# Kernel optimization log

Measured on AMD Instinct MI355X. Metric: run time of the kernel, lower is better.

The kernel has to match this reference:

```python
import jax, jax.numpy as jnp
import numpy as np

BN_EPS = 1e-5


def gcn_conv(x, src, dst, n, W, b):
    # PyG GCNConv: h = x @ W; add self-loops; symmetric deg^{-1/2} norm; scatter-add; + bias
    h = x @ W
    sl = jnp.arange(n, dtype=src.dtype)
    src_f = jnp.concatenate([src, sl])
    dst_f = jnp.concatenate([dst, sl])
    deg = jax.ops.segment_sum(jnp.ones_like(dst_f, dtype=h.dtype), dst_f, num_segments=n)
    dis = jnp.where(deg > 0, jax.lax.rsqrt(jnp.maximum(deg, 1.0)), 0.0)
    norm = dis[src_f] * dis[dst_f]                       # [E+N]
    msg = h[src_f] * norm[:, None]                       # gather + scale
    out = jax.ops.segment_sum(msg, dst_f, num_segments=n)  # scatter-add
    return out + b


def batchnorm(x, g, b):
    # training-mode BatchNorm1d (batch statistics), deterministic
    mu = jnp.mean(x, axis=0)
    var = jnp.mean((x - mu) ** 2, axis=0)
    return g * (x - mu) * jax.lax.rsqrt(var + BN_EPS) + b


def setup_inputs() -> dict:
    key = jax.random.key(0)
    ks = jax.random.split(key, 12)
    N, E, F_IN, D, M, G = 40000, 640000, 128, 128, 256, 2000
    x = jax.random.normal(ks[0], (N, F_IN), dtype=jnp.float32)
    edge_index = jax.random.randint(ks[1], (2, E), 0, N, dtype=jnp.int64)
    batch = jnp.sort(jax.random.randint(ks[2], (N,), 0, G, dtype=jnp.int64))
    s = lambda fi: 1.0 / np.sqrt(fi)
    W1 = jax.random.normal(ks[3], (F_IN, D), dtype=jnp.float32) * s(F_IN)
    b1 = jnp.zeros((D,), jnp.float32)
    W2 = jax.random.normal(ks[4], (D, D), dtype=jnp.float32) * s(D)
    b2 = jnp.zeros((D,), jnp.float32)
    bn1_g = jnp.ones((D,), jnp.float32); bn1_b = jnp.zeros((D,), jnp.float32)
    bn2_g = jnp.ones((D,), jnp.float32); bn2_b = jnp.zeros((D,), jnp.float32)
    fc1_w = jax.random.normal(ks[5], (D, M), dtype=jnp.float32) * s(D)
    fc1_b = jnp.zeros((M,), jnp.float32)
    fc2_w = jax.random.normal(ks[6], (M, M), dtype=jnp.float32) * s(M)
    fc2_b = jnp.zeros((M,), jnp.float32)
    fc3_w = jax.random.normal(ks[7], (M, 1), dtype=jnp.float32) * s(M)
    fc3_b = jnp.zeros((1,), jnp.float32)
    return dict(x=x, edge_index=edge_index, batch=batch, num_graphs=G,
                W1=W1, b1=b1, W2=W2, b2=b2,
                bn1_g=bn1_g, bn1_b=bn1_b, bn2_g=bn2_g, bn2_b=bn2_b,
                fc1_w=fc1_w, fc1_b=fc1_b, fc2_w=fc2_w, fc2_b=fc2_b,
                fc3_w=fc3_w, fc3_b=fc3_b)


def reference(x, edge_index, batch, num_graphs, W1, b1, W2, b2,
              bn1_g, bn1_b, bn2_g, bn2_b,
              fc1_w, fc1_b, fc2_w, fc2_b, fc3_w, fc3_b):
    n = x.shape[0]
    src, dst = edge_index[0], edge_index[1]
    h = gcn_conv(x, src, dst, n, W1, b1)
    h = jax.nn.relu(batchnorm(h, bn1_g, bn1_b))
    h = gcn_conv(h, src, dst, n, W2, b2)
    h = jax.nn.relu(batchnorm(h, bn2_g, bn2_b))
    g = jax.ops.segment_sum(h, batch, num_segments=num_graphs)  # scatter_sum pooling [G, D]
    g = jax.nn.relu(g @ fc1_w + fc1_b)   # dropout is identity in eval
    g = jax.nn.relu(g @ fc2_w + fc2_b)
    return g @ fc3_w + fc3_b             # [G, 1]
```

## Files before the change

kernel.cpp:

```cpp
#include <hip/hip_runtime.h>
#include <hip/hip_fp16.h>

#define NN 40000
#define NE 640000
#define DF 128
#define NG 2000
#define NCH 157
#define FILLB 625
#define G1_BLKS 313
#define NCHUNK 64
#define ECH 10000
#define NOCT 8
#define QN 5120
#define NPAD (NOCT * QN)
#define NWIN 160
#define HISTB (NCHUNK * NOCT)

typedef unsigned int u32;
typedef __attribute__((ext_vector_type(8))) short short8;
typedef __attribute__((ext_vector_type(4))) float floatx4;

__device__ inline float2 bf2_to_f2(u32 u) {
    return make_float2(__uint_as_float(u << 16), __uint_as_float(u & 0xffff0000u));
}
__device__ inline u32 f_to_bf(float f) {
    u32 u = __float_as_uint(f);
    return (u + 0x7fffu + ((u >> 16) & 1u)) >> 16;
}
__device__ inline u32 pack_bf2(float a, float b) {
    return f_to_bf(a) | (f_to_bf(b) << 16);
}
__device__ inline float bf_to_f(short s) {
    return __uint_as_float(((u32)(unsigned short)s) << 16);
}
__device__ inline float colw_to_f(int cw) {
    return __half2float(__ushort_as_half((unsigned short)((u32)cw >> 16)));
}

template<bool BF16IN, bool FUSE_BN, bool WT_F32, bool TILE128>
__device__ __forceinline__ void gemm_core(const void* __restrict__ Xv, const void* __restrict__ wsrc,
                                          u32* __restrict__ outb, const float* __restrict__ slots,
                                          const float* __restrict__ gam, const float* __restrict__ bet,
                                          int bid, char* sbuf, float* sc, float* sh) {
    unsigned short* wlds = (unsigned short*)sbuf;
    unsigned short* clds = (unsigned short*)sbuf;
    int tid = threadIdx.x;
    int row0 = bid * (TILE128 ? 128 : 64);

    if (FUSE_BN) {
        if (tid < 128) {
            float s = 0.f, q = 0.f;
            for (int k = 0; k < 64; k++) {
                s += slots[k * 256 + tid];
                q += slots[k * 256 + 128 + tid];
            }
            const float inv_n = 1.0f / (float)NN;
            float mu = s * inv_n;
            float va = fmaf(-mu, mu, q * inv_n);
            float a = gam[tid] * rsqrtf(va + 1e-5f);
            sc[tid] = a;
            sh[tid] = fmaf(-mu, a, bet[tid]);
        }
    }
    if (WT_F32) {
        const float* W = (const float*)wsrc;
        for (int i = tid; i < 16384; i += 256) {
            int k = i >> 7, c = i & 127;
            wlds[c * 136 + k] = (unsigned short)f_to_bf(W[i]);
        }
    } else {
        const unsigned short* wt = (const unsigned short*)wsrc;
        for (int i = tid; i < 2048; i += 256) {
            int c = i >> 4, s = i & 15;
            *(uint4*)&wlds[c * 136 + s * 8] = ((const uint4*)wt)[i];
        }
    }
    __syncthreads();

    int lane = tid & 63;
    int wave = tid >> 6;
    int qr = lane >> 4;
    int rl = lane & 15;

    if (TILE128) {
        int rA0 = row0 + wave * 32 + rl;
        int rA1 = rA0 + 16;
        int rA0c = rA0 < NN ? rA0 : NN - 1;
        int rA1c = rA1 < NN ? rA1 : NN - 1;
        floatx4 acc[2][8];
#pragma unroll
        for (int a = 0; a < 2; a++)
#pragma unroll
            for (int b = 0; b < 8; b++) acc[a][b] = (floatx4){0.f, 0.f, 0.f, 0.f};
#pragma unroll
        for (int kb = 0; kb < 4; kb++) {
            int k0 = kb * 32 + qr * 8;
            short8 a0, a1;
            if (!BF16IN) {
                const float* p0 = (const float*)Xv + (size_t)rA0c * DF + k0;
                const float* p1 = (const float*)Xv + (size_t)rA1c * DF + k0;
                float4 u0 = *(const float4*)p0, u1 = *(const float4*)(p0 + 4);
                float4 v0 = *(const float4*)p1, v1 = *(const float4*)(p1 + 4);
                float fa[8] = {u0.x, u0.y, u0.z, u0.w, u1.x, u1.y, u1.z, u1.w};
                float fb[8] = {v0.x, v0.y, v0.z, v0.w, v1.x, v1.y, v1.z, v1.w};
#pragma unroll
                for (int j = 0; j < 8; j++) { a0[j] = (short)f_to_bf(fa[j]); a1[j] = (short)f_to_bf(fb[j]); }
            } else {
                a0 = *(const short8*)((const u32*)Xv + (size_t)rA0c * 64 + (k0 >> 1));
                a1 = *(const short8*)((const u32*)Xv + (size_t)rA1c * 64 + (k0 >> 1));
                if (FUSE_BN) {
#pragma unroll
                    for (int j = 0; j < 8; j++) {
                        float f0 = fmaxf(fmaf(bf_to_f(a0[j]), sc[k0 + j], sh[k0 + j]), 0.f);
                        float f1 = fmaxf(fmaf(bf_to_f(a1[j]), sc[k0 + j], sh[k0 + j]), 0.f);
                        a0[j] = (short)f_to_bf(f0);
                        a1[j] = (short)f_to_bf(f1);
                    }
                }
            }
#pragma unroll
            for (int ct = 0; ct < 8; ct++) {
                short8 bfr = *(const short8*)&wlds[(ct * 16 + rl) * 136 + k0];
                acc[0][ct] = __builtin_amdgcn_mfma_f32_16x16x32_bf16(a0, bfr, acc[0][ct], 0, 0, 0);
                acc[1][ct] = __builtin_amdgcn_mfma_f32_16x16x32_bf16(a1, bfr, acc[1][ct], 0, 0, 0);
            }
        }
        __syncthreads();
#pragma unroll
        for (int rt = 0; rt < 2; rt++)
#pragma unroll
            for (int ct = 0; ct < 8; ct++)
#pragma unroll
                for (int r = 0; r < 4; r++) {
                    int lr = wave * 32 + rt * 16 + qr * 4 + r;
                    int c = ct * 16 + rl;
                    clds[lr * 136 + c] = (unsigned short)f_to_bf(acc[rt][ct][r]);
                }
        __syncthreads();
        for (int i = tid; i < 2048; i += 256) {
            int lr = i >> 4, s = i & 15;
            int grow = row0 + lr;
            if (grow < NN) {
                uint4 v = *(const uint4*)&clds[lr * 136 + s * 8];
                ((uint4*)(outb + (size_t)grow * 64))[s] = v;
            }
        }
    } else {
        int rA = row0 + wave * 16 + rl;
        floatx4 acc[8];
#pragma unroll
        for (int b = 0; b < 8; b++) acc[b] = (floatx4){0.f, 0.f, 0.f, 0.f};
#pragma unroll
        for (int kb = 0; kb < 4; kb++) {
            int k0 = kb * 32 + qr * 8;
            short8 a0;
            if (!BF16IN) {
                const float* p0 = (const float*)Xv + (size_t)rA * DF + k0;
                float4 u0 = *(const float4*)p0, u1 = *(const float4*)(p0 + 4);
                float fa[8] = {u0.x, u0.y, u0.z, u0.w, u1.x, u1.y, u1.z, u1.w};
#pragma unroll
                for (int j = 0; j < 8; j++) a0[j] = (short)f_to_bf(fa[j]);
            } else {
                a0 = *(const short8*)((const u32*)Xv + (size_t)rA * 64 + (k0 >> 1));
                if (FUSE_BN) {
#pragma unroll
                    for (int j = 0; j < 8; j++) {
                        float f0 = fmaxf(fmaf(bf_to_f(a0[j]), sc[k0 + j], sh[k0 + j]), 0.f);
                        a0[j] = (short)f_to_bf(f0);
                    }
                }
            }
#pragma unroll
            for (int ct = 0; ct < 8; ct++) {
                short8 bfr = *(const short8*)&wlds[(ct * 16 + rl) * 136 + k0];
                acc[ct] = __builtin_amdgcn_mfma_f32_16x16x32_bf16(a0, bfr, acc[ct], 0, 0, 0);
            }
        }
        __syncthreads();
#pragma unroll
        for (int ct = 0; ct < 8; ct++)
#pragma unroll
            for (int r = 0; r < 4; r++) {
                int lr = wave * 16 + qr * 4 + r;
                int c = ct * 16 + rl;
                clds[lr * 136 + c] = (unsigned short)f_to_bf(acc[ct][r]);
            }
        __syncthreads();
        for (int i = tid; i < 1024; i += 256) {
            int lr = i >> 4, s = i & 15;
            uint4 v = *(const uint4*)&clds[lr * 136 + s * 8];
            ((uint4*)(outb + (size_t)(row0 + lr) * 64))[s] = v;
        }
    }
}

__global__ __launch_bounds__(256, 4) void k_countgemm(const int* __restrict__ dst,
                                                      int* __restrict__ degT, int* __restrict__ rank,
                                                      int* __restrict__ wsum, float* __restrict__ slots0,
                                                      const float* __restrict__ W1, const float* __restrict__ W2,
                                                      unsigned short* __restrict__ wt2,
                                                      const float* __restrict__ X, u32* __restrict__ outb) {
    __shared__ __align__(16) char sbuf[34816];
    __shared__ float sc[128], sh[128];
    int bid = blockIdx.x;
    int tid = threadIdx.x;
    if (bid < HISTB) {
        int c = bid >> 3, oct = bid & 7;
        int nlo = oct * QN;
        int* hist = (int*)sbuf;
        for (int i = tid; i < QN; i += 256) hist[i] = 0;
        __syncthreads();
        int ebase = c * ECH;
        for (int i = tid; i < ECH; i += 256) {
            int d = dst[ebase + i];
            int t = d - nlo;
            if ((u32)t < (u32)QN) rank[ebase + i] = atomicAdd(&hist[t], 1);
        }
        __syncthreads();
        for (int i = tid; i < QN; i += 256) degT[(size_t)c * NPAD + nlo + i] = hist[i];
        int wv = tid >> 6, lane = tid & 63;
        for (int lw = wv; lw < 20; lw += 4) {
            int v = hist[lw * 256 + lane] + hist[lw * 256 + 64 + lane]
                  + hist[lw * 256 + 128 + lane] + hist[lw * 256 + 192 + lane];
            for (int off = 32; off > 0; off >>= 1) v += __shfl_down(v, off);
            if (lane == 0) wsum[c * NWIN + oct * 20 + lw] = v;
        }
        return;
    }
    if (bid < HISTB + 2) {
        float* s = slots0 + (size_t)(bid - HISTB) * 64 * 256;
        for (int i = tid; i < 64 * 256; i += 256) s[i] = 0.f;
        return;
    }
    if (bid == HISTB + 2) {
        for (int i = tid; i < 128 * 128; i += 256) {
            int k = i >> 7, cc = i & 127;
            wt2[cc * 128 + k] = (unsigned short)f_to_bf(W2[i]);
        }
        return;
    }
    gemm_core<false, false, true, true>(X, W1, outb, nullptr, nullptr, nullptr,
                                        bid - HISTB - 3, sbuf, sc, sh);
}

__global__ __launch_bounds__(256) void k_scan(const int* __restrict__ degT, const int* __restrict__ wsum,
                                              int* __restrict__ baseT,
                                              int* __restrict__ row_ptr, float* __restrict__ dis) {
    __shared__ int red[256];
    __shared__ int ls[256];
    int tid = threadIdx.x;
    int wnd = blockIdx.x;
    int part = 0;
    int wp = tid < NWIN ? tid : tid - NWIN;
    for (int idx = tid; idx < NCHUNK * NWIN; idx += 256) {
        if (wp < wnd) part += wsum[idx];
        wp += 96; if (wp >= NWIN) wp -= NWIN;
    }
    red[tid] = part;
    int n = wnd * 256 + tid;
    int run = 0;
#pragma unroll 4
    for (int c = 0; c < NCHUNK; c++) {
        int v = degT[(size_t)c * NPAD + n];
        baseT[(size_t)c * NPAD + n] = run;
        run += v;
    }
    int d = run;
    ls[tid] = d;
    __syncthreads();
#pragma unroll
    for (int off = 128; off > 0; off >>= 1) {
        if (tid < off) red[tid] += red[tid + off];
        __syncthreads();
    }
    int base = red[0];
#pragma unroll
    for (int off = 1; off < 256; off <<= 1) {
        int t = (tid >= off) ? ls[tid - off] : 0;
        __syncthreads();
        ls[tid] += t;
        __syncthreads();
    }
    if (n < NN) {
        int r = base + ls[tid] - d;
        row_ptr[n] = r;
        dis[n] = rsqrtf((float)(d + 1));
    }
    if (wnd == NCH - 1 && tid == 0) row_ptr[NN] = NE;
}

__global__ __launch_bounds__(256) void k_fill(const int* __restrict__ src, const int* __restrict__ dst,
                                              const int* __restrict__ rank, const int* __restrict__ row_ptr,
                                              const int* __restrict__ baseT,
                                              const float* __restrict__ dis, u32* __restrict__ col) {
    int e0 = blockIdx.x * 1024 + threadIdx.x;
#pragma unroll
    for (int q = 0; q < 4; q++) {
        int e = e0 + q * 256;
        int d = dst[e];
        int s = src[e];
        int r = rank[e];
        int c = e / ECH;
        u32 h = (u32)__half_as_ushort(__float2half(dis[s]));
        col[row_ptr[d] + baseT[(size_t)c * NPAD + d] + r] = (u32)s | (h << 16);
    }
}

__global__ __launch_bounds__(256, 4) void k_gemm2(const u32* __restrict__ Hb, const unsigned short* __restrict__ wt2,
                                                  u32* __restrict__ outb, const float* __restrict__ slots,
                                                  const float* __restrict__ gam, const float* __restrict__ bet) {
    __shared__ __align__(16) char sbuf[34816];
    __shared__ float sc[128], sh[128];
    gemm_core<true, true, false, true>(Hb, wt2, outb, slots, gam, bet, blockIdx.x, sbuf, sc, sh);
}

__global__ __launch_bounds__(256, 8) void k_gather(const u32* __restrict__ Hb, const int* __restrict__ row_ptr,
                                                   const u32* __restrict__ col, const float* __restrict__ dis,
                                                   const float* __restrict__ bias, u32* __restrict__ outb,
                                                   float* __restrict__ slots) {
    __shared__ float sred[4][128];
    __shared__ float qred[4][128];
    int t = threadIdx.x & 63;
    int wv = threadIdx.x >> 6;
    int node = blockIdx.x * 4 + wv;
    float di = dis[node];
    int lo = row_ptr[node], hi = row_ptr[node + 1];
    float2 acc;
    {
        float2 a = bf2_to_f2(Hb[(size_t)node * 64 + t]);
        float s = di * di;
        acc = make_float2(a.x * s, a.y * s);
    }
    for (int base = lo; base < hi; base += 64) {
        int m = hi - base; if (m > 64) m = 64;
        int cw = 0;
        if (t < m) cw = (int)col[base + t];
        int ng = (m + 3) >> 2;
        int c[4]; u32 u[4];
#pragma unroll
        for (int q = 0; q < 4; q++) {
            int idx = q < m ? q : 0;
            c[q] = __shfl(cw, idx);
            u[q] = Hb[(size_t)(c[q] & 0xffff) * 64 + t];
        }
        for (int g = 1; g < ng; g++) {
            int c2[4]; u32 u2[4];
#pragma unroll
            for (int q = 0; q < 4; q++) {
                int ii = g * 4 + q;
                int idx = ii < m ? ii : 0;
                c2[q] = __shfl(cw, idx);
                u2[q] = Hb[(size_t)(c2[q] & 0xffff) * 64 + t];
            }
#pragma unroll
            for (int q = 0; q < 4; q++) {
                int ii = (g - 1) * 4 + q;
                float wq = ii < m ? di * colw_to_f(c[q]) : 0.f;
                float2 h = bf2_to_f2(u[q]);
                acc.x = fmaf(h.x, wq, acc.x);
                acc.y = fmaf(h.y, wq, acc.y);
            }
#pragma unroll
            for (int q = 0; q < 4; q++) { c[q] = c2[q]; u[q] = u2[q]; }
        }
#pragma unroll
        for (int q = 0; q < 4; q++) {
            int ii = (ng - 1) * 4 + q;
            float wq = ii < m ? di * colw_to_f(c[q]) : 0.f;
            float2 h = bf2_to_f2(u[q]);
            acc.x = fmaf(h.x, wq, acc.x);
            acc.y = fmaf(h.y, wq, acc.y);
        }
    }
    float2 b = ((const float2*)bias)[t];
    acc.x += b.x; acc.y += b.y;
    outb[(size_t)node * 64 + t] = pack_bf2(acc.x, acc.y);
    sred[wv][2 * t] = acc.x;     sred[wv][2 * t + 1] = acc.y;
    qred[wv][2 * t] = acc.x * acc.x; qred[wv][2 * t + 1] = acc.y * acc.y;
    __syncthreads();
    int tid = threadIdx.x;
    if (tid < 128) {
        float s = sred[0][tid] + sred[1][tid] + sred[2][tid] + sred[3][tid];
        float q = qred[0][tid] + qred[1][tid] + qred[2][tid] + qred[3][tid];
        int slot = blockIdx.x & 63;
        atomicAdd(&slots[slot * 256 + tid], s);
        atomicAdd(&slots[slot * 256 + 128 + tid], q);
    }
}

__global__ __launch_bounds__(256) void k_poolfc(const u32* __restrict__ Hb, const int* __restrict__ batch,
                                                const float* __restrict__ slots,
                                                const float* __restrict__ gam, const float* __restrict__ bet,
                                                const float* __restrict__ fc1w, const float* __restrict__ fc1b,
                                                const float* __restrict__ fc2w, const float* __restrict__ fc2b,
                                                const float* __restrict__ fc3w, const float* __restrict__ fc3b,
                                                float* __restrict__ out) {
    __shared__ float sc[128], sh[128];
    __shared__ float pooled[4][128];
    __shared__ float g1[4][256];
    __shared__ float g2[4][256];
    __shared__ int bnds[5];
    int tid = threadIdx.x;
    int gbase = blockIdx.x * 4;
    if (tid < 128) {
        float s = 0.f, q = 0.f;
        for (int k = 0; k < 64; k++) {
            s += slots[k * 256 + tid];
            q += slots[k * 256 + 128 + tid];
        }
        const float inv_n = 1.0f / (float)NN;
        float mu = s * inv_n;
        float va = fmaf(-mu, mu, q * inv_n);
        float a = gam[tid] * rsqrtf(va + 1e-5f);
        sc[tid] = a;
        sh[tid] = fmaf(-mu, a, bet[tid]);
    } else if (tid < 133) {
        int target = gbase + (tid - 128);
        int a = 0, b = NN;
        while (a < b) { int m = (a + b) >> 1; if (batch[m] < target) a = m + 1; else b = m; }
        bnds[tid - 128] = a;
    }
    __syncthreads();
    {
        int g = tid >> 6, p = tid & 63;
        int lo = bnds[g], hi = bnds[g + 1];
        float a0 = 0.f, a1 = 0.f;
        float sc0 = sc[2 * p], sh0 = sh[2 * p], sc1 = sc[2 * p + 1], sh1 = sh[2 * p + 1];
        for (int i = lo; i < hi; i++) {
            float2 v = bf2_to_f2(Hb[(size_t)i * 64 + p]);
            a0 += fmaxf(fmaf(v.x, sc0, sh0), 0.f);
            a1 += fmaxf(fmaf(v.y, sc1, sh1), 0.f);
        }
        pooled[g][2 * p] = a0;
        pooled[g][2 * p + 1] = a1;
    }
    __syncthreads();
    {
        float x0 = 0.f, x1 = 0.f, x2 = 0.f, x3 = 0.f;
        for (int k = 0; k < 128; k++) {
            float wv = fc1w[k * 256 + tid];
            x0 = fmaf(pooled[0][k], wv, x0);
            x1 = fmaf(pooled[1][k], wv, x1);
            x2 = fmaf(pooled[2][k], wv, x2);
            x3 = fmaf(pooled[3][k], wv, x3);
        }
        float bb = fc1b[tid];
        g1[0][tid] = fmaxf(x0 + bb, 0.f);
        g1[1][tid] = fmaxf(x1 + bb, 0.f);
        g1[2][tid] = fmaxf(x2 + bb, 0.f);
        g1[3][tid] = fmaxf(x3 + bb, 0.f);
    }
    __syncthreads();
    {
        float x0 = 0.f, x1 = 0.f, x2 = 0.f, x3 = 0.f;
        for (int k = 0; k < 256; k++) {
            float wv = fc2w[k * 256 + tid];
            x0 = fmaf(g1[0][k], wv, x0);
            x1 = fmaf(g1[1][k], wv, x1);
            x2 = fmaf(g1[2][k], wv, x2);
            x3 = fmaf(g1[3][k], wv, x3);
        }
        float bb = fc2b[tid];
        g2[0][tid] = fmaxf(x0 + bb, 0.f);
        g2[1][tid] = fmaxf(x1 + bb, 0.f);
        g2[2][tid] = fmaxf(x2 + bb, 0.f);
        g2[3][tid] = fmaxf(x3 + bb, 0.f);
    }
    __syncthreads();
    {
        int lane = tid & 63, wv = tid >> 6;
        float s = fmaf(g2[wv][lane], fc3w[lane],
                  fmaf(g2[wv][64 + lane], fc3w[64 + lane],
                  fmaf(g2[wv][128 + lane], fc3w[128 + lane],
                       g2[wv][192 + lane] * fc3w[192 + lane])));
        for (int off = 32; off > 0; off >>= 1) s += __shfl_down(s, off);
        if (lane == 0) out[gbase + wv] = s + fc3b[0];
    }
}

extern "C" void kernel_launch(void* const* d_in, const int* in_sizes, int n_in,
                              void* d_out, int out_size, void* d_ws, size_t ws_size,
                              hipStream_t stream) {
    const float* x    = (const float*)d_in[0];
    const int*   ei   = (const int*)d_in[1];
    const int*   batch= (const int*)d_in[2];
    const float* W1   = (const float*)d_in[4];
    const float* b1   = (const float*)d_in[5];
    const float* W2   = (const float*)d_in[6];
    const float* b2   = (const float*)d_in[7];
    const float* bn1g = (const float*)d_in[8];
    const float* bn1b = (const float*)d_in[9];
    const float* bn2g = (const float*)d_in[10];
    const float* bn2b = (const float*)d_in[11];
    const float* fc1w = (const float*)d_in[12];
    const float* fc1b = (const float*)d_in[13];
    const float* fc2w = (const float*)d_in[14];
    const float* fc2b = (const float*)d_in[15];
    const float* fc3w = (const float*)d_in[16];
    const float* fc3b = (const float*)d_in[17];
    const int* src = ei;
    const int* dst = ei + NE;
    float* outp = (float*)d_out;

    char* w = (char*)d_ws;
    size_t o = 0;
    auto alloc = [&](size_t bytes) -> char* {
        char* p = w + o;
        o = (o + bytes + 255) & ~(size_t)255;
        return p;
    };
    int*   degT    = (int*)alloc((size_t)NCHUNK * NPAD * 4);
    int*   baseT   = (int*)alloc((size_t)NCHUNK * NPAD * 4);
    int*   wsum    = (int*)alloc((size_t)NCHUNK * NWIN * 4);
    float* slots0  = (float*)alloc((size_t)2 * 64 * 256 * 4);
    int*   row_ptr = (int*)alloc((size_t)(NN + 1) * 4);
    int*   rank    = (int*)alloc((size_t)NE * 4);
    u32*   col     = (u32*)alloc((size_t)NE * 4);
    float* dis     = (float*)alloc((size_t)NN * 4);
    unsigned short* wt2 = (unsigned short*)alloc(128 * 128 * 2);
    u32*   bufA    = (u32*)alloc((size_t)NN * 64 * 4);
    u32*   bufB    = (u32*)alloc((size_t)NN * 64 * 4);
    float* slotsA  = slots0;
    float* slotsB  = slots0 + 64 * 256;

    k_countgemm<<<HISTB + 3 + G1_BLKS, 256, 0, stream>>>(dst, degT, rank, wsum, slots0,
                                                         W1, W2, wt2, x, bufA);
    k_scan<<<NCH, 256, 0, stream>>>(degT, wsum, baseT, row_ptr, dis);
    k_fill<<<FILLB, 256, 0, stream>>>(src, dst, rank, row_ptr, baseT, dis, col);
    k_gather<<<NN / 4, 256, 0, stream>>>(bufA, row_ptr, col, dis, b1, bufB, slotsA);
    k_gemm2<<<G1_BLKS, 256, 0, stream>>>(bufB, wt2, bufA, slotsA, bn1g, bn1b);
    k_gather<<<NN / 4, 256, 0, stream>>>(bufA, row_ptr, col, dis, b2, bufB, slotsB);
    k_poolfc<<<NG / 4, 256, 0, stream>>>(bufB, batch, slotsB, bn2g, bn2b,
                                         fc1w, fc1b, fc2w, fc2b, fc3w, fc3b, outp);
}
```

Before: 261.6 us.

## Replace chunked histogram CSR build with global atomic degree count and cursor fill

Replaces the per-chunk shared-memory histograms (degT/baseT/rank/wsum) with a single global atomic degree count, a simple prefix scan over degrees, and a fill pass that claims CSR slots by atomically bumping per-node cursors. This drops the large 64x40960 intermediate arrays and the per-edge rank buffer, cutting memory traffic in the scan and fill stages. The cost is global atomic contention and a non-deterministic neighbour order within each CSR row, which can change floating-point summation order. The gather also folds the destination-side normalization into a single final multiply instead of scaling every edge weight.

```diff
diff --git a/kernel.cpp b/kernel.cpp
--- a/kernel.cpp
+++ b/kernel.cpp
@@ -6,15 +6,9 @@
 #define DF 128
 #define NG 2000
 #define NCH 157
-#define FILLB 625
+#define CNTB 625
 #define G1_BLKS 313
-#define NCHUNK 64
-#define ECH 10000
-#define NOCT 8
-#define QN 5120
-#define NPAD (NOCT * QN)
-#define NWIN 160
-#define HISTB (NCHUNK * NOCT)
+#define NDPAD 40192
 
 typedef unsigned int u32;
 typedef __attribute__((ext_vector_type(8))) short short8;
@@ -195,8 +189,7 @@
 }
 
 __global__ __launch_bounds__(256, 4) void k_countgemm(const int* __restrict__ dst,
-                                                      int* __restrict__ degT, int* __restrict__ rank,
-                                                      int* __restrict__ wsum, float* __restrict__ slots0,
+                                                      int* __restrict__ deg, float* __restrict__ slots0,
                                                       const float* __restrict__ W1, const float* __restrict__ W2,
                                                       unsigned short* __restrict__ wt2,
                                                       const float* __restrict__ X, u32* __restrict__ outb) {
@@ -204,35 +197,21 @@
     __shared__ float sc[128], sh[128];
     int bid = blockIdx.x;
     int tid = threadIdx.x;
-    if (bid < HISTB) {
-        int c = bid >> 3, oct = bid & 7;
-        int nlo = oct * QN;
-        int* hist = (int*)sbuf;
-        for (int i = tid; i < QN; i += 256) hist[i] = 0;
-        __syncthreads();
-        int ebase = c * ECH;
-        for (int i = tid; i < ECH; i += 256) {
-            int d = dst[ebase + i];
-            int t = d - nlo;
-            if ((u32)t < (u32)QN) rank[ebase + i] = atomicAdd(&hist[t], 1);
-        }
-        __syncthreads();
-        for (int i = tid; i < QN; i += 256) degT[(size_t)c * NPAD + nlo + i] = hist[i];
-        int wv = tid >> 6, lane = tid & 63;
-        for (int lw = wv; lw < 20; lw += 4) {
-            int v = hist[lw * 256 + lane] + hist[lw * 256 + 64 + lane]
-                  + hist[lw * 256 + 128 + lane] + hist[lw * 256 + 192 + lane];
-            for (int off = 32; off > 0; off >>= 1) v += __shfl_down(v, off);
-            if (lane == 0) wsum[c * NWIN + oct * 20 + lw] = v;
-        }
+    if (bid < CNTB) {
+        int i4 = bid * 256 + tid;
+        int4 d4 = ((const int4*)dst)[i4];
+        atomicAdd(&deg[d4.x], 1);
+        atomicAdd(&deg[d4.y], 1);
+        atomicAdd(&deg[d4.z], 1);
+        atomicAdd(&deg[d4.w], 1);
         return;
     }
-    if (bid < HISTB + 2) {
-        float* s = slots0 + (size_t)(bid - HISTB) * 64 * 256;
+    if (bid < CNTB + 2) {
+        float* s = slots0 + (size_t)(bid - CNTB) * 64 * 256;
         for (int i = tid; i < 64 * 256; i += 256) s[i] = 0.f;
         return;
     }
-    if (bid == HISTB + 2) {
+    if (bid == CNTB + 2) {
         for (int i = tid; i < 128 * 128; i += 256) {
             int k = i >> 7, cc = i & 127;
             wt2[cc * 128 + k] = (unsigned short)f_to_bf(W2[i]);
@@ -240,32 +219,22 @@
         return;
     }
     gemm_core<false, false, true, true>(X, W1, outb, nullptr, nullptr, nullptr,
-                                        bid - HISTB - 3, sbuf, sc, sh);
-}
-
-__global__ __launch_bounds__(256) void k_scan(const int* __restrict__ degT, const int* __restrict__ wsum,
-                                              int* __restrict__ baseT,
-                                              int* __restrict__ row_ptr, float* __restrict__ dis) {
+                                        bid - CNTB - 3, sbuf, sc, sh);
+}
+
+__global__ __launch_bounds__(256) void k_scan(const int* __restrict__ deg,
+                                              int* __restrict__ row_ptr, int* __restrict__ curs,
+                                              float* __restrict__ dis) {
     __shared__ int red[256];
     __shared__ int ls[256];
     int tid = threadIdx.x;
     int wnd = blockIdx.x;
     int part = 0;
-    int wp = tid < NWIN ? tid : tid - NWIN;
-    for (int idx = tid; idx < NCHUNK * NWIN; idx += 256) {
-        if (wp < wnd) part += wsum[idx];
-        wp += 96; if (wp >= NWIN) wp -= NWIN;
-    }
+    int lim = wnd * 256;
+    for (int idx = tid; idx < lim; idx += 256) part += deg[idx];
     red[tid] = part;
-    int n = wnd * 256 + tid;
-    int run = 0;
-#pragma unroll 4
-    for (int c = 0; c < NCHUNK; c++) {
-        int v = degT[(size_t)c * NPAD + n];
-        baseT[(size_t)c * NPAD + n] = run;
-        run += v;
-    }
-    int d = run;
+    int n = lim + tid;
+    int d = deg[n];
     ls[tid] = d;
     __syncthreads();
 #pragma unroll
@@ -284,25 +253,25 @@
     if (n < NN) {
         int r = base + ls[tid] - d;
         row_ptr[n] = r;
+        curs[n] = r;
         dis[n] = rsqrtf((float)(d + 1));
     }
     if (wnd == NCH - 1 && tid == 0) row_ptr[NN] = NE;
 }
 
 __global__ __launch_bounds__(256) void k_fill(const int* __restrict__ src, const int* __restrict__ dst,
-                                              const int* __restrict__ rank, const int* __restrict__ row_ptr,
-                                              const int* __restrict__ baseT,
+                                              int* __restrict__ curs,
                                               const float* __restrict__ dis, u32* __restrict__ col) {
-    int e0 = blockIdx.x * 1024 + threadIdx.x;
+    int i4 = blockIdx.x * 256 + threadIdx.x;
+    int4 d4 = ((const int4*)dst)[i4];
+    int4 s4 = ((const int4*)src)[i4];
+    int dd[4] = {d4.x, d4.y, d4.z, d4.w};
+    int ss[4] = {s4.x, s4.y, s4.z, s4.w};
 #pragma unroll
     for (int q = 0; q < 4; q++) {
-        int e = e0 + q * 256;
-        int d = dst[e];
-        int s = src[e];
-        int r = rank[e];
-        int c = e / ECH;
-        u32 h = (u32)__half_as_ushort(__float2half(dis[s]));
-        col[row_ptr[d] + baseT[(size_t)c * NPAD + d] + r] = (u32)s | (h << 16);
+        u32 h = (u32)__half_as_ushort(__float2half(dis[ss[q]]));
+        int slot = atomicAdd(&curs[dd[q]], 1);
+        col[slot] = (u32)ss[q] | (h << 16);
     }
 }
 
@@ -328,8 +297,7 @@
     float2 acc;
     {
         float2 a = bf2_to_f2(Hb[(size_t)node * 64 + t]);
-        float s = di * di;
-        acc = make_float2(a.x * s, a.y * s);
+        acc = make_float2(a.x * di, a.y * di);
     }
     for (int base = lo; base < hi; base += 64) {
         int m = hi - base; if (m > 64) m = 64;
@@ -355,7 +323,7 @@
 #pragma unroll
             for (int q = 0; q < 4; q++) {
                 int ii = (g - 1) * 4 + q;
-                float wq = ii < m ? di * colw_to_f(c[q]) : 0.f;
+                float wq = ii < m ? colw_to_f(c[q]) : 0.f;
                 float2 h = bf2_to_f2(u[q]);
                 acc.x = fmaf(h.x, wq, acc.x);
                 acc.y = fmaf(h.y, wq, acc.y);
@@ -366,14 +334,15 @@
 #pragma unroll
         for (int q = 0; q < 4; q++) {
             int ii = (ng - 1) * 4 + q;
-            float wq = ii < m ? di * colw_to_f(c[q]) : 0.f;
+            float wq = ii < m ? colw_to_f(c[q]) : 0.f;
             float2 h = bf2_to_f2(u[q]);
             acc.x = fmaf(h.x, wq, acc.x);
             acc.y = fmaf(h.y, wq, acc.y);
         }
     }
     float2 b = ((const float2*)bias)[t];
-    acc.x += b.x; acc.y += b.y;
+    acc.x = fmaf(acc.x, di, b.x);
+    acc.y = fmaf(acc.y, di, b.y);
     outb[(size_t)node * 64 + t] = pack_bf2(acc.x, acc.y);
     sred[wv][2 * t] = acc.x;     sred[wv][2 * t + 1] = acc.y;
     qred[wv][2 * t] = acc.x * acc.x; qred[wv][2 * t + 1] = acc.y * acc.y;
@@ -509,12 +478,10 @@
         o = (o + bytes + 255) & ~(size_t)255;
         return p;
     };
-    int*   degT    = (int*)alloc((size_t)NCHUNK * NPAD * 4);
-    int*   baseT   = (int*)alloc((size_t)NCHUNK * NPAD * 4);
-    int*   wsum    = (int*)alloc((size_t)NCHUNK * NWIN * 4);
+    int*   deg     = (int*)alloc((size_t)NDPAD * 4);
+    int*   curs    = (int*)alloc((size_t)NDPAD * 4);
     float* slots0  = (float*)alloc((size_t)2 * 64 * 256 * 4);
     int*   row_ptr = (int*)alloc((size_t)(NN + 1) * 4);
-    int*   rank    = (int*)alloc((size_t)NE * 4);
     u32*   col     = (u32*)alloc((size_t)NE * 4);
     float* dis     = (float*)alloc((size_t)NN * 4);
     unsigned short* wt2 = (unsigned short*)alloc(128 * 128 * 2);
@@ -523,10 +490,10 @@
     float* slotsA  = slots0;
     float* slotsB  = slots0 + 64 * 256;
 
-    k_countgemm<<<HISTB + 3 + G1_BLKS, 256, 0, stream>>>(dst, degT, rank, wsum, slots0,
-                                                         W1, W2, wt2, x, bufA);
-    k_scan<<<NCH, 256, 0, stream>>>(degT, wsum, baseT, row_ptr, dis);
-    k_fill<<<FILLB, 256, 0, stream>>>(src, dst, rank, row_ptr, baseT, dis, col);
+    hipMemsetAsync(deg, 0, (size_t)NDPAD * 4, stream);
+    k_countgemm<<<CNTB + 3 + G1_BLKS, 256, 0, stream>>>(dst, deg, slots0, W1, W2, wt2, x, bufA);
+    k_scan<<<NCH, 256, 0, stream>>>(deg, row_ptr, curs, dis);
+    k_fill<<<CNTB, 256, 0, stream>>>(src, dst, curs, dis, col);
     k_gather<<<NN / 4, 256, 0, stream>>>(bufA, row_ptr, col, dis, b1, bufB, slotsA);
     k_gemm2<<<G1_BLKS, 256, 0, stream>>>(bufB, wt2, bufA, slotsA, bn1g, bn1b);
     k_gather<<<NN / 4, 256, 0, stream>>>(bufA, row_ptr, col, dis, b2, bufB, slotsB);
```

After: 287.9 us. +10.0%, slower.
